# Optimization experiments

Hardware: AMD Instinct MI355X
Metric: run time of the kernel (lower is better)

Reference implementation:

```python
import jax, jax.numpy as jnp
import numpy as np

EPS = 1e-5

def _ln(v, gamma, beta):
    mu = jnp.mean(v, axis=-1, keepdims=True)
    var = jnp.mean(jnp.square(v - mu), axis=-1, keepdims=True)
    return (v - mu) * jax.lax.rsqrt(var + EPS) * gamma + beta

def setup_inputs() -> dict:
    B, T, D = 8, 2048, 2048
    NG = 3  # n_strands - 1
    key = jax.random.key(0)
    ks = jax.random.split(key, 8)
    s = lambda k, shp, fan: jax.random.normal(k, shp, jnp.float32) * (1.0 / np.sqrt(fan))
    return {
        "x": jax.random.normal(ks[0], (B, T, D), jnp.float32),
        "W1": s(ks[1], (D, 2 * D), 2 * D), "b1": jnp.zeros((D,), jnp.float32),
        "W2": s(ks[2], (2 * NG, D), D), "b2": jnp.zeros((2 * NG,), jnp.float32),
        "Wp": s(ks[3], (D, D), D), "bp": jnp.zeros((D,), jnp.float32),
        "gamma": jnp.ones((D,), jnp.float32), "beta": jnp.zeros((D,), jnp.float32),
    }

def reference(x, W1, b1, W2, b2, Wp, bp, gamma, beta):
    # Adjacent-pair crossing features: pair_t = [x_t, x_{t+1}], t = 0..T-2
    pair = jnp.concatenate([x[:, :-1], x[:, 1:]], axis=-1)          # (B,T-1,2D)
    h = jax.nn.gelu(jnp.einsum('btk,dk->btd', pair, W1) + b1, approximate=False)
    logits = jnp.einsum('btd,gd->btg', h, W2) + b2                   # (B,T-1,2*NG)
    scale = jnp.mean(jax.nn.softmax(logits, axis=-1), axis=-1, keepdims=True)  # (B,T-1,1)
    P = jnp.einsum('btd,ed->bte', x, Wp) + bp                        # mix_proj(x)
    m = P[:, 1:] * scale    # added to position t at step t
    mp = P[:, :-1] * scale  # added to position t+1 at step t
    # Loop semantics: pos t first updated as j at step t-1, then as i at step t.
    tmp = jnp.concatenate([x[:, :1], _ln(x[:, 1:] + mp, gamma, beta)], axis=1)
    out = jnp.concatenate([_ln(tmp[:, :-1] + m, gamma, beta), tmp[:, -1:]], axis=1)
    return out
```

## Files before the change

kernel.cpp:

```cpp
#include <hip/hip_runtime.h>
#include <stdint.h>


#define B_DIM 8
#define T_DIM 2048
#define D_DIM 2048
#define M_DIM (B_DIM * T_DIM)
#define N_DIM D_DIM
#define K_DIM D_DIM
#define LROWS 8

typedef __attribute__((ext_vector_type(8))) short short8;
typedef __attribute__((ext_vector_type(4))) float f32x4;

__device__ inline unsigned short f2bf(float f) {
    unsigned u = __float_as_uint(f);
    u += 0x7fffu + ((u >> 16) & 1u);
    return (unsigned short)(u >> 16);
}
__device__ inline float bf2f(unsigned u16) {
    return __uint_as_float(u16 << 16);
}
__device__ inline void unpack8(uint4 u, float* f) {
    f[0] = bf2f(u.x & 0xffffu); f[1] = bf2f(u.x >> 16);
    f[2] = bf2f(u.y & 0xffffu); f[3] = bf2f(u.y >> 16);
    f[4] = bf2f(u.z & 0xffffu); f[5] = bf2f(u.z >> 16);
    f[6] = bf2f(u.w & 0xffffu); f[7] = bf2f(u.w >> 16);
}
__device__ inline void async_ld16(const void* g, void* l) {
    __builtin_amdgcn_global_load_lds(
        (__attribute__((address_space(1))) void*)(g),
        (__attribute__((address_space(3))) void*)(l),
        16, 0, 0);
}

__global__ void cast_f32_bf16(const float* __restrict__ x, unsigned short* __restrict__ Xb,
                              const float* __restrict__ Wp, unsigned short* __restrict__ Wb,
                              int nx4, int ntot4) {
    for (int i = blockIdx.x * blockDim.x + threadIdx.x; i < ntot4;
         i += gridDim.x * blockDim.x) {
        const float* src; unsigned short* dst; int j;
        if (i < nx4) { src = x; dst = Xb; j = i; }
        else         { src = Wp; dst = Wb; j = i - nx4; }
        float4 f = ((const float4*)src)[j];
        ushort4 o;
        o.x = f2bf(f.x); o.y = f2bf(f.y); o.z = f2bf(f.z); o.w = f2bf(f.w);
        ((ushort4*)dst)[j] = o;
    }
}

__global__ void gemm_bt(const unsigned short* __restrict__ Xb,
                        const unsigned short* __restrict__ Wb,
                        const float* __restrict__ bp,
                        unsigned short* __restrict__ P)
{
    __shared__ unsigned short As[128 * 64];
    __shared__ unsigned short Bs[128 * 64];

    const int tid  = threadIdx.x;
    const int lane = tid & 63;
    const int wave = tid >> 6;
    const int m0 = blockIdx.y * 128;
    const int n0 = blockIdx.x * 128;

    const int rw = (wave >> 1) * 64;
    const int cw = (wave & 1) * 64;
    const int fr = lane & 15;
    const int lq = lane >> 4;

    int s_r[4], s_l[4], s_ci[4];
#pragma unroll
    for (int q = 0; q < 4; q++) {
        int ci = (wave * 4 + q) * 64 + lane;
        s_ci[q] = ci;
        s_r[q] = ci >> 3;
        s_l[q] = (ci & 7) ^ (s_r[q] & 7);
    }

    f32x4 acc[4][4];
#pragma unroll
    for (int i = 0; i < 4; i++)
#pragma unroll
        for (int j = 0; j < 4; j++) acc[i][j] = (f32x4){0.f, 0.f, 0.f, 0.f};

    for (int k0 = 0; k0 < K_DIM; k0 += 64) {
#pragma unroll
        for (int q = 0; q < 4; q++) {
            async_ld16(Xb + (size_t)(m0 + s_r[q]) * K_DIM + k0 + s_l[q] * 8,
                       As + s_ci[q] * 8);
            async_ld16(Wb + (size_t)(n0 + s_r[q]) * K_DIM + k0 + s_l[q] * 8,
                       Bs + s_ci[q] * 8);
        }
        __syncthreads();

#pragma unroll
        for (int kk = 0; kk < 2; kk++) {
            const int l = kk * 4 + lq;
            short8 a[4], b[4];
#pragma unroll
            for (int i = 0; i < 4; i++) {
                int row = rw + 16 * i + fr;
                a[i] = *(const short8*)(As + row * 64 + (l ^ (row & 7)) * 8);
            }
#pragma unroll
            for (int j = 0; j < 4; j++) {
                int row = cw + 16 * j + fr;
                b[j] = *(const short8*)(Bs + row * 64 + (l ^ (row & 7)) * 8);
            }
#pragma unroll
            for (int i = 0; i < 4; i++)
#pragma unroll
                for (int j = 0; j < 4; j++)
                    acc[i][j] = __builtin_amdgcn_mfma_f32_16x16x32_bf16(a[i], b[j], acc[i][j], 0, 0, 0);
        }
        __syncthreads();
    }

    const int crow = (lane >> 4) * 4;
    const int ccol = lane & 15;
    float bpv[4];
#pragma unroll
    for (int j = 0; j < 4; j++) bpv[j] = bp[n0 + cw + 16 * j + ccol];
#pragma unroll
    for (int i = 0; i < 4; i++) {
#pragma unroll
        for (int r = 0; r < 4; r++) {
            size_t base = (size_t)(m0 + rw + 16 * i + crow + r) * N_DIM
                        + n0 + cw + ccol;
#pragma unroll
            for (int j = 0; j < 4; j++)
                P[base + 16 * j] = f2bf(acc[i][j][r] + bpv[j]);
        }
    }
}

__device__ __attribute__((always_inline)) inline
void ln_wave(float (&v)[32], const float (&g)[32], const float (&be)[32], int lane) {
    float s = 0.f, q = 0.f;
#pragma unroll
    for (int i = 0; i < 32; ++i) { s += v[i]; q += v[i] * v[i]; }
#pragma unroll
    for (int off = 32; off; off >>= 1) {
        s += __shfl_xor(s, off);
        q += __shfl_xor(q, off);
    }
    const float invD = 1.0f / (float)D_DIM;
    const float mu = s * invD;
    const float rs = rsqrtf(q * invD - mu * mu + 1e-5f);
#pragma unroll
    for (int i = 0; i < 32; ++i) v[i] = (v[i] - mu) * rs * g[i] + be[i];
}

__global__ __launch_bounds__(256, 2)
void ln_kernel(const unsigned short* __restrict__ Xb,
               const unsigned short* __restrict__ P,
               const float* __restrict__ gamma,
               const float* __restrict__ beta,
               float* __restrict__ out)
{
    const int lane = threadIdx.x & 63;
    const int w = blockIdx.x * 4 + (threadIdx.x >> 6);
    const int r0 = w * LROWS;
    const int t0 = r0 & (T_DIM - 1);
    const float inv6 = 1.0f / 6.0f;

    float g[32], be[32];
    {
        const float4* g4 = (const float4*)gamma;
        const float4* b4 = (const float4*)beta;
#pragma unroll
        for (int c = 0; c < 4; ++c) {
            const int e = (c * 64 + lane) * 2;
            float4 g0 = g4[e], g1 = g4[e + 1];
            float4 b0 = b4[e], b1 = b4[e + 1];
            g[c*8+0]=g0.x; g[c*8+1]=g0.y; g[c*8+2]=g0.z; g[c*8+3]=g0.w;
            g[c*8+4]=g1.x; g[c*8+5]=g1.y; g[c*8+6]=g1.z; g[c*8+7]=g1.w;
            be[c*8+0]=b0.x; be[c*8+1]=b0.y; be[c*8+2]=b0.z; be[c*8+3]=b0.w;
            be[c*8+4]=b1.x; be[c*8+5]=b1.y; be[c*8+6]=b1.z; be[c*8+7]=b1.w;
        }
    }

    const uint4* Pq = (const uint4*)P;
    uint4 pm[4], pc[4], pn[4];
    {
        const int rm = (t0 > 0) ? r0 - 1 : r0;
#pragma unroll
        for (int c = 0; c < 4; ++c) pm[c] = Pq[(size_t)rm * 256 + c * 64 + lane];
#pragma unroll
        for (int c = 0; c < 4; ++c) pc[c] = Pq[(size_t)r0 * 256 + c * 64 + lane];
    }

    for (int tt = 0; tt < LROWS; ++tt) {
        const int r = r0 + tt;
        const int t = t0 + tt;

        const int rn = (t < T_DIM - 1) ? r + 1 : r;
#pragma unroll
        for (int c = 0; c < 4; ++c) pn[c] = Pq[(size_t)rn * 256 + c * 64 + lane];

        float v[32];
        const uint4* xq = (const uint4*)Xb + (size_t)r * 256;
#pragma unroll
        for (int c = 0; c < 4; ++c) {
            float f[8]; unpack8(xq[c * 64 + lane], f);
#pragma unroll
            for (int jj = 0; jj < 8; ++jj) v[c * 8 + jj] = f[jj];
        }

        if (t > 0) {
#pragma unroll
            for (int c = 0; c < 4; ++c) {
                float f[8]; unpack8(pm[c], f);
#pragma unroll
                for (int jj = 0; jj < 8; ++jj) v[c * 8 + jj] += f[jj] * inv6;
            }
            ln_wave(v, g, be, lane);
        }
        if (t < T_DIM - 1) {
#pragma unroll
            for (int c = 0; c < 4; ++c) {
                float f[8]; unpack8(pn[c], f);
#pragma unroll
                for (int jj = 0; jj < 8; ++jj) v[c * 8 + jj] += f[jj] * inv6;
            }
            ln_wave(v, g, be, lane);
        }

        float4* orow = (float4*)(out + (size_t)r * D_DIM);
#pragma unroll
        for (int c = 0; c < 4; ++c) {
            const int e = (c * 64 + lane) * 2;
            orow[e]     = (float4){v[c*8+0], v[c*8+1], v[c*8+2], v[c*8+3]};
            orow[e + 1] = (float4){v[c*8+4], v[c*8+5], v[c*8+6], v[c*8+7]};
        }

#pragma unroll
        for (int c = 0; c < 4; ++c) { pm[c] = pc[c]; pc[c] = pn[c]; }
    }
}

extern "C" void kernel_launch(void* const* d_in, const int* in_sizes, int n_in,
                              void* d_out, int out_size, void* d_ws, size_t ws_size,
                              hipStream_t stream) {
    const float* x     = (const float*)d_in[0];
    const float* Wp    = (const float*)d_in[5];
    const float* bp    = (const float*)d_in[6];
    const float* gamma = (const float*)d_in[7];
    const float* beta  = (const float*)d_in[8];
    float* out = (float*)d_out;

    unsigned short* Xb = (unsigned short*)d_ws;
    unsigned short* Wb = Xb + (size_t)M_DIM * K_DIM;
    unsigned short* P  = Wb + (size_t)N_DIM * K_DIM;

    const int nx4   = (M_DIM * K_DIM) / 4;
    const int ntot4 = nx4 + (N_DIM * K_DIM) / 4;
    cast_f32_bf16<<<4096, 256, 0, stream>>>(x, Xb, Wp, Wb, nx4, ntot4);

    dim3 ggrid(N_DIM / 128, M_DIM / 128);
    gemm_bt<<<ggrid, 256, 0, stream>>>(Xb, Wb, bp, P);

    ln_kernel<<<(M_DIM / LROWS) / 4, 256, 0, stream>>>(Xb, P, gamma, beta, out);
}
```

Before: 426.6 us.

## Use one row per wave in LN kernel and split GEMM into two launches

The LayerNorm kernel now gives each wave a single row instead of eight, so it launches eight times as many blocks. Gamma and beta are reloaded from global memory inside each normalization instead of being held in registers, and the two-blocks-per-SM launch bound is dropped. The GEMM is split into two half-M launches via a row offset. The aim is more parallelism and lower register pressure in the LN pass, at the cost of reloading each P row about three times instead of once and an extra kernel launch.

```diff
diff --git a/kernel.cpp b/kernel.cpp
--- a/kernel.cpp
+++ b/kernel.cpp
@@ -8,7 +8,6 @@
 #define M_DIM (B_DIM * T_DIM)
 #define N_DIM D_DIM
 #define K_DIM D_DIM
-#define LROWS 8
 
 typedef __attribute__((ext_vector_type(8))) short short8;
 typedef __attribute__((ext_vector_type(4))) float f32x4;
@@ -52,7 +51,8 @@
 __global__ void gemm_bt(const unsigned short* __restrict__ Xb,
                         const unsigned short* __restrict__ Wb,
                         const float* __restrict__ bp,
-                        unsigned short* __restrict__ P)
+                        unsigned short* __restrict__ P,
+                        int moff)
 {
     __shared__ unsigned short As[128 * 64];
     __shared__ unsigned short Bs[128 * 64];
@@ -60,7 +60,7 @@
     const int tid  = threadIdx.x;
     const int lane = tid & 63;
     const int wave = tid >> 6;
-    const int m0 = blockIdx.y * 128;
+    const int m0 = moff + blockIdx.y * 128;
     const int n0 = blockIdx.x * 128;
 
     const int rw = (wave >> 1) * 64;
@@ -135,7 +135,8 @@
 }
 
 __device__ __attribute__((always_inline)) inline
-void ln_wave(float (&v)[32], const float (&g)[32], const float (&be)[32], int lane) {
+void ln_wave(float (&v)[32], const float* __restrict__ gamma,
+             const float* __restrict__ beta, int lane) {
     float s = 0.f, q = 0.f;
 #pragma unroll
     for (int i = 0; i < 32; ++i) { s += v[i]; q += v[i] * v[i]; }
@@ -147,11 +148,25 @@
     const float invD = 1.0f / (float)D_DIM;
     const float mu = s * invD;
     const float rs = rsqrtf(q * invD - mu * mu + 1e-5f);
-#pragma unroll
-    for (int i = 0; i < 32; ++i) v[i] = (v[i] - mu) * rs * g[i] + be[i];
-}
-
-__global__ __launch_bounds__(256, 2)
+    const float4* g4 = (const float4*)gamma;
+    const float4* b4 = (const float4*)beta;
+#pragma unroll
+    for (int c = 0; c < 4; ++c) {
+        const int e = (c * 64 + lane) * 2;
+        float4 g0 = g4[e], g1 = g4[e + 1];
+        float4 b0 = b4[e], b1 = b4[e + 1];
+        v[c*8+0] = (v[c*8+0] - mu) * rs * g0.x + b0.x;
+        v[c*8+1] = (v[c*8+1] - mu) * rs * g0.y + b0.y;
+        v[c*8+2] = (v[c*8+2] - mu) * rs * g0.z + b0.z;
+        v[c*8+3] = (v[c*8+3] - mu) * rs * g0.w + b0.w;
+        v[c*8+4] = (v[c*8+4] - mu) * rs * g1.x + b1.x;
+        v[c*8+5] = (v[c*8+5] - mu) * rs * g1.y + b1.y;
+        v[c*8+6] = (v[c*8+6] - mu) * rs * g1.z + b1.z;
+        v[c*8+7] = (v[c*8+7] - mu) * rs * g1.w + b1.w;
+    }
+}
+
+__global__ __launch_bounds__(256)
 void ln_kernel(const unsigned short* __restrict__ Xb,
                const unsigned short* __restrict__ P,
                const float* __restrict__ gamma,
@@ -159,83 +174,56 @@
                float* __restrict__ out)
 {
     const int lane = threadIdx.x & 63;
-    const int w = blockIdx.x * 4 + (threadIdx.x >> 6);
-    const int r0 = w * LROWS;
-    const int t0 = r0 & (T_DIM - 1);
+    const int r = blockIdx.x * 4 + (threadIdx.x >> 6);
+    const int t = r & (T_DIM - 1);
     const float inv6 = 1.0f / 6.0f;
 
-    float g[32], be[32];
-    {
-        const float4* g4 = (const float4*)gamma;
-        const float4* b4 = (const float4*)beta;
+    const uint4* xq = (const uint4*)Xb + (size_t)r * 256;
+    const uint4* Pq = (const uint4*)P;
+    const int rm = (t > 0) ? r - 1 : r;
+    const int rn = (t < T_DIM - 1) ? r + 1 : r;
+
+    uint4 xr[4], pmr[4], pnr[4];
+#pragma unroll
+    for (int c = 0; c < 4; ++c) xr[c]  = xq[c * 64 + lane];
+#pragma unroll
+    for (int c = 0; c < 4; ++c) pmr[c] = Pq[(size_t)rm * 256 + c * 64 + lane];
+#pragma unroll
+    for (int c = 0; c < 4; ++c) pnr[c] = Pq[(size_t)rn * 256 + c * 64 + lane];
+
+    float v[32];
+#pragma unroll
+    for (int c = 0; c < 4; ++c) {
+        float f[8]; unpack8(xr[c], f);
+#pragma unroll
+        for (int jj = 0; jj < 8; ++jj) v[c * 8 + jj] = f[jj];
+    }
+
+    if (t > 0) {
 #pragma unroll
         for (int c = 0; c < 4; ++c) {
-            const int e = (c * 64 + lane) * 2;
-            float4 g0 = g4[e], g1 = g4[e + 1];
-            float4 b0 = b4[e], b1 = b4[e + 1];
-            g[c*8+0]=g0.x; g[c*8+1]=g0.y; g[c*8+2]=g0.z; g[c*8+3]=g0.w;
-            g[c*8+4]=g1.x; g[c*8+5]=g1.y; g[c*8+6]=g1.z; g[c*8+7]=g1.w;
-            be[c*8+0]=b0.x; be[c*8+1]=b0.y; be[c*8+2]=b0.z; be[c*8+3]=b0.w;
-            be[c*8+4]=b1.x; be[c*8+5]=b1.y; be[c*8+6]=b1.z; be[c*8+7]=b1.w;
-        }
-    }
-
-    const uint4* Pq = (const uint4*)P;
-    uint4 pm[4], pc[4], pn[4];
-    {
-        const int rm = (t0 > 0) ? r0 - 1 : r0;
-#pragma unroll
-        for (int c = 0; c < 4; ++c) pm[c] = Pq[(size_t)rm * 256 + c * 64 + lane];
-#pragma unroll
-        for (int c = 0; c < 4; ++c) pc[c] = Pq[(size_t)r0 * 256 + c * 64 + lane];
-    }
-
-    for (int tt = 0; tt < LROWS; ++tt) {
-        const int r = r0 + tt;
-        const int t = t0 + tt;
-
-        const int rn = (t < T_DIM - 1) ? r + 1 : r;
-#pragma unroll
-        for (int c = 0; c < 4; ++c) pn[c] = Pq[(size_t)rn * 256 + c * 64 + lane];
-
-        float v[32];
-        const uint4* xq = (const uint4*)Xb + (size_t)r * 256;
+            float f[8]; unpack8(pmr[c], f);
+#pragma unroll
+            for (int jj = 0; jj < 8; ++jj) v[c * 8 + jj] += f[jj] * inv6;
+        }
+        ln_wave(v, gamma, beta, lane);
+    }
+    if (t < T_DIM - 1) {
 #pragma unroll
         for (int c = 0; c < 4; ++c) {
-            float f[8]; unpack8(xq[c * 64 + lane], f);
-#pragma unroll
-            for (int jj = 0; jj < 8; ++jj) v[c * 8 + jj] = f[jj];
-        }
-
-        if (t > 0) {
-#pragma unroll
-            for (int c = 0; c < 4; ++c) {
-                float f[8]; unpack8(pm[c], f);
-#pragma unroll
-                for (int jj = 0; jj < 8; ++jj) v[c * 8 + jj] += f[jj] * inv6;
-            }
-            ln_wave(v, g, be, lane);
-        }
-        if (t < T_DIM - 1) {
-#pragma unroll
-            for (int c = 0; c < 4; ++c) {
-                float f[8]; unpack8(pn[c], f);
-#pragma unroll
-                for (int jj = 0; jj < 8; ++jj) v[c * 8 + jj] += f[jj] * inv6;
-            }
-            ln_wave(v, g, be, lane);
-        }
-
-        float4* orow = (float4*)(out + (size_t)r * D_DIM);
-#pragma unroll
-        for (int c = 0; c < 4; ++c) {
-            const int e = (c * 64 + lane) * 2;
-            orow[e]     = (float4){v[c*8+0], v[c*8+1], v[c*8+2], v[c*8+3]};
-            orow[e + 1] = (float4){v[c*8+4], v[c*8+5], v[c*8+6], v[c*8+7]};
-        }
-
-#pragma unroll
-        for (int c = 0; c < 4; ++c) { pm[c] = pc[c]; pc[c] = pn[c]; }
+            float f[8]; unpack8(pnr[c], f);
+#pragma unroll
+            for (int jj = 0; jj < 8; ++jj) v[c * 8 + jj] += f[jj] * inv6;
+        }
+        ln_wave(v, gamma, beta, lane);
+    }
+
+    float4* orow = (float4*)(out + (size_t)r * D_DIM);
+#pragma unroll
+    for (int c = 0; c < 4; ++c) {
+        const int e = (c * 64 + lane) * 2;
+        orow[e]     = (float4){v[c*8+0], v[c*8+1], v[c*8+2], v[c*8+3]};
+        orow[e + 1] = (float4){v[c*8+4], v[c*8+5], v[c*8+6], v[c*8+7]};
     }
 }
 
@@ -257,8 +245,9 @@
     const int ntot4 = nx4 + (N_DIM * K_DIM) / 4;
     cast_f32_bf16<<<4096, 256, 0, stream>>>(x, Xb, Wp, Wb, nx4, ntot4);
 
-    dim3 ggrid(N_DIM / 128, M_DIM / 128);
-    gemm_bt<<<ggrid, 256, 0, stream>>>(Xb, Wb, bp, P);
-
-    ln_kernel<<<(M_DIM / LROWS) / 4, 256, 0, stream>>>(Xb, P, gamma, beta, out);
-}
+    dim3 ggrid(N_DIM / 128, M_DIM / 256);
+    gemm_bt<<<ggrid, 256, 0, stream>>>(Xb, Wb, bp, P, 0);
+    gemm_bt<<<ggrid, 256, 0, stream>>>(Xb, Wb, bp, P, M_DIM / 2);
+
+    ln_kernel<<<M_DIM / 4, 256, 0, stream>>>(Xb, P, gamma, beta, out);
+}
```

Measured after the change: 430.5 us. Within noise of the previous version (+0.9%).
